# Performance work log

Measured on AMD Instinct MI355X. Metric: run time of the kernel, lower is better.

The kernel has to match this reference:

```python
import jax, jax.numpy as jnp
import numpy as np

B, T = 8, 512
N_QUBITS, N_ROT, D_PER = 64, 16, 64
D = N_QUBITS * D_PER


def setup_inputs() -> dict:
    key = jax.random.key(0)
    k1, k2, k3, k4 = jax.random.split(key, 4)
    return {
        "x": jax.random.normal(k1, (B, T, D), dtype=jnp.float32),
        "rx_params": jax.random.normal(k2, (N_QUBITS, N_ROT), dtype=jnp.float32),
        "ry_params": jax.random.normal(k3, (N_QUBITS, N_ROT), dtype=jnp.float32),
        "rz_params": jax.random.normal(k4, (N_QUBITS, N_ROT), dtype=jnp.float32),
    }


def _rot_diag(theta, axis):
    # theta: (Q,) per-qubit angle. The torch einsum 'btqd,btqq->btqd' only uses
    # the diagonal of the (Q,Q) rotation matrix. For rx/ry, the paired-qubit
    # construction puts cos(theta_k/2) on both diagonal slots of pair k
    # (first Q//2 angles are used, matching cos[..., :len(idx)]).
    Q = theta.shape[0]
    half = theta[: Q // 2] * 0.5
    if axis in ("x", "y"):
        return jnp.repeat(jnp.cos(half).astype(jnp.complex64), 2)
    # rz: diag(exp(-i a/2), exp(+i a/2)) interleaved over pairs
    e = jnp.exp(-1j * half.astype(jnp.complex64))
    return jnp.stack([e, jnp.conj(e)], axis=-1).reshape(-1)


def _apply_rotation(state, theta, axis):
    # state: (B, T, Q, d_per) complex64
    sf = jnp.fft.fft2(state, axes=(-2, -1))
    sf = sf * _rot_diag(theta, axis)[:, None]  # diagonal per-qubit scale
    return jnp.fft.ifft2(sf, axes=(-2, -1)).real  # torch takes .real


def reference(x, rx_params, ry_params, rz_params):
    b, t, d = x.shape
    q = rx_params.shape[0]
    state = x.reshape(b, t, q, d // q).astype(jnp.complex64)
    for params, axis in ((rx_params, "x"), (ry_params, "y"), (rz_params, "z")):
        theta = params.sum(-1)  # combine n_rotations into one angle per qubit
        state = _apply_rotation(state, theta, axis).astype(jnp.complex64)
    state = state.reshape(b, t, d)
    # noise model: (1 + amp_noise) * exp(i * phase_noise) * state, then L2 norm
    ka, kp = jax.random.split(jax.random.key(42))
    amp = 0.01 * jax.random.normal(ka, state.shape, dtype=jnp.float32)
    ph = 0.005 * jax.random.normal(kp, state.shape, dtype=jnp.float32)
    noisy = (1.0 + amp) * jnp.exp(1j * ph.astype(jnp.complex64)) * state
    norm = jnp.linalg.norm(noisy, axis=-1, keepdims=True)
    noisy = noisy / (norm + 1e-8)
    return jnp.abs(noisy)  # measurement
```

## Files before the change

kernel.cpp:

```cpp
#include <hip/hip_runtime.h>
#include <stdint.h>

typedef _Float16 half8 __attribute__((ext_vector_type(8)));
typedef float floatx4 __attribute__((ext_vector_type(4)));

__device__ __forceinline__ uint32_t rotl32(uint32_t v, int r) {
  return __builtin_amdgcn_alignbit(v, v, 32 - r);
}

__device__ __forceinline__ void threefry2x32(uint32_t k0, uint32_t k1,
                                             uint32_t x0, uint32_t x1,
                                             uint32_t& o0, uint32_t& o1) {
  uint32_t k2 = k0 ^ k1 ^ 0x1BD11BDAu;
  x0 += k0; x1 += k1;
#define TF_R(r) { x0 += x1; x1 = rotl32(x1, (r)); x1 ^= x0; }
  TF_R(13) TF_R(15) TF_R(26) TF_R(6)   x0 += k1; x1 += k2 + 1u;
  TF_R(17) TF_R(29) TF_R(16) TF_R(24)  x0 += k2; x1 += k0 + 2u;
  TF_R(13) TF_R(15) TF_R(26) TF_R(6)   x0 += k0; x1 += k1 + 3u;
  TF_R(17) TF_R(29) TF_R(16) TF_R(24)  x0 += k1; x1 += k2 + 4u;
  TF_R(13) TF_R(15) TF_R(26) TF_R(6)   x0 += k2; x1 += k0 + 5u;
#undef TF_R
  o0 = x0; o1 = x1;
}

__device__ __forceinline__ void threefry4x(uint32_t ka0, uint32_t ka1,
                                           const uint32_t idx[4],
                                           uint32_t bits[4]) {
  const uint32_t k2 = ka0 ^ ka1 ^ 0x1BD11BDAu;
  uint32_t x0[4], x1[4];
#pragma unroll
  for (int i = 0; i < 4; ++i) { x0[i] = ka0; x1[i] = idx[i] + ka1; }
#define TF_RND(r)                                                     \
  _Pragma("unroll") for (int i = 0; i < 4; ++i) {                     \
    x0[i] += x1[i]; x1[i] = rotl32(x1[i], (r)); x1[i] ^= x0[i];       \
  }
#define TF_INJ(a, b, c)                                               \
  _Pragma("unroll") for (int i = 0; i < 4; ++i) {                     \
    x0[i] += (a); x1[i] += (b) + (c);                                 \
  }
  TF_RND(13) TF_RND(15) TF_RND(26) TF_RND(6)   TF_INJ(ka1, k2, 1u)
  TF_RND(17) TF_RND(29) TF_RND(16) TF_RND(24)  TF_INJ(k2, ka0, 2u)
  TF_RND(13) TF_RND(15) TF_RND(26) TF_RND(6)   TF_INJ(ka0, ka1, 3u)
  TF_RND(17) TF_RND(29) TF_RND(16) TF_RND(24)  TF_INJ(ka1, k2, 4u)
  TF_RND(13) TF_RND(15) TF_RND(26) TF_RND(6)   TF_INJ(k2, ka0, 5u)
#undef TF_RND
#undef TF_INJ
#pragma unroll
  for (int i = 0; i < 4; ++i) bits[i] = x0[i] ^ x1[i];
}

__device__ __forceinline__ float tail_p(float l2) {
  float w = l2 * -0.69314718f;
  float s = sqrtf(w) - 3.0f;
  float p = -0.000200214257f;
  p = fmaf(p, s, 0.000100950558f);
  p = fmaf(p, s, 0.00134934322f);
  p = fmaf(p, s, -0.00367342844f);
  p = fmaf(p, s, 0.00573950773f);
  p = fmaf(p, s, -0.0076224613f);
  p = fmaf(p, s, 0.00943887047f);
  p = fmaf(p, s, 1.00167406f);
  p = fmaf(p, s, 2.83297682f);
  return p;
}

__device__ __forceinline__ void noise4(uint32_t ka0, uint32_t ka1,
                                       const uint32_t idx[4], float nm[4]) {
  uint32_t bits[4];
  threefry4x(ka0, ka1, idx, bits);
  float u[4], l2[4], p[4];
#pragma unroll
  for (int i = 0; i < 4; ++i) {
    float vf = __uint_as_float(__builtin_amdgcn_alignbit(0x7Fu, bits[i], 9));
    u[i] = fmaxf(fmaf(vf, 2.0f, -3.0f), -0.99999994f);
    float t = fmaf(-u[i], u[i], 1.0f);
    l2[i] = __log2f(t);
  }
#pragma unroll
  for (int i = 0; i < 4; ++i) {
    float a = fmaf(l2[i], -0.69314718f, -2.5f);
    float q = fmaf(-0.00417768164f, a, 0.246640727f);
    p[i] = fmaf(q, a, 1.50140941f);
  }
  const float lmin = fminf(fminf(l2[0], l2[1]), fminf(l2[2], l2[3]));
  if (__builtin_expect(lmin <= -7.2134752f, 0)) {
#pragma unroll
    for (int i = 0; i < 4; ++i)
      if (l2[i] <= -7.2134752f) p[i] = tail_p(l2[i]);
  }
#pragma unroll
  for (int i = 0; i < 4; ++i)
    nm[i] = fmaf(p[i], u[i] * 0.014142135623730951f, 1.0f);
}

__device__ __align__(16) _Float16 g_afrag[256 * 16];
__device__ uint32_t g_key[2];

__global__ void setup_kernel(const float* __restrict__ rx,
                             const float* __restrict__ ry,
                             const float* __restrict__ rz) {
  __shared__ float cre[3][64], cim[3][64];
  __shared__ float Gr[64], Gi[64];
  __shared__ float twc[64], tws[64];
  __shared__ float gs[64];
  const int t = threadIdx.x;

  if (t < 32) {
    const float* ps[3] = {rx, ry, rz};
    for (int a = 0; a < 3; ++a) {
      float s = 0.0f;
      for (int r = 0; r < 16; ++r) s += ps[a][t * 16 + r];
      float h = 0.5f * s;
      float ch = cosf(h), sh = sinf(h);
      if (a < 2) {
        cre[a][2 * t] = ch;     cim[a][2 * t] = 0.0f;
        cre[a][2 * t + 1] = ch; cim[a][2 * t + 1] = 0.0f;
      } else {
        cre[2][2 * t] = ch;     cim[2][2 * t] = -sh;
        cre[2][2 * t + 1] = ch; cim[2][2 * t + 1] = sh;
      }
    }
  }
  if (t < 64) {
    double ang = (2.0 * 3.14159265358979323846 / 64.0) * (double)t;
    twc[t] = (float)cos(ang);
    tws[t] = (float)sin(ang);
  }
  __syncthreads();

  if (t < 64) {
    const int k = t, kn = (64 - k) & 63;
    float pr = 1.0f, pi = 0.0f;
    for (int a = 0; a < 3; ++a) {
      float cr = 0.5f * (cre[a][k] + cre[a][kn]);
      float ci = 0.5f * (cim[a][k] - cim[a][kn]);
      float nr = pr * cr - pi * ci;
      float ni = pr * ci + pi * cr;
      pr = nr; pi = ni;
    }
    Gr[k] = pr; Gi[k] = pi;
  }
  __syncthreads();

  if (t < 64) {
    const int mi = t;
    float s = 0.0f;
    for (int k = 0; k < 64; ++k) {
      int idx = (k * mi) & 63;
      s = fmaf(Gr[k], twc[idx], s);
      s = fmaf(-Gi[k], tws[idx], s);
    }
    gs[mi] = s * (1.0f / 64.0f);
  }
  __syncthreads();

  {
    const int w = t >> 6, lane = t & 63, quad = lane >> 4, m = lane & 15;
    const int r0 = 16 * w + m - 8 * quad;
#pragma unroll
    for (int j = 0; j < 8; ++j) {
      g_afrag[t * 16 + j]     = (_Float16)gs[(r0 - j) & 63];
      g_afrag[t * 16 + 8 + j] = (_Float16)gs[(r0 - 32 - j) & 63];
    }
  }

  if (t == 0) {
    uint32_t o0, o1;
    threefry2x32(0u, 42u, 0u, 0u, o0, o1);
    g_key[0] = o0; g_key[1] = o1;
  }
}

__global__ __launch_bounds__(512, 6) void qmain(const float* __restrict__ x,
                                                float* __restrict__ out) {
  __shared__ __align__(16) _Float16 Xt[64 * 72];
  __shared__ float red[8];
  const int tid = threadIdx.x;
  const int row = blockIdx.x;
  const int lane = tid & 63;
  const int w = tid >> 6;
  const int wr = w & 3;
  const int wc = w >> 2;
  const int quad = lane >> 4;
  const int m = lane & 15;

  const half8* at = (const half8*)g_afrag;
  const int ai = (wr << 6) | lane;
  half8 af0 = at[2 * ai];
  half8 af1 = at[2 * ai + 1];
  const uint32_t ka0 = g_key[0], ka1 = g_key[1];

  {
    const float* xr = x + (size_t)row * 4096;
    const int d0 = (tid & 31) * 2;
    const int q0 = (tid >> 5) * 4;
    float2 v[4];
#pragma unroll
    for (int s = 0; s < 4; ++s) v[s] = *(const float2*)(xr + (q0 + s) * 64 + d0);
    union { _Float16 h[4]; uint2 u; } r0, r1;
#pragma unroll
    for (int s = 0; s < 4; ++s) { r0.h[s] = (_Float16)v[s].x; r1.h[s] = (_Float16)v[s].y; }
    *(uint2*)&Xt[d0 * 72 + q0] = r0.u;
    *(uint2*)&Xt[(d0 + 1) * 72 + q0] = r1.u;
  }
  __syncthreads();

  floatx4 acc[2];
#pragma unroll
  for (int cc = 0; cc < 2; ++cc) {
    const int c = 2 * wc + cc;
    const _Float16* bp = &Xt[(16 * c + m) * 72 + 8 * quad];
    half8 b0 = *(const half8*)bp;
    half8 b1 = *(const half8*)(bp + 32);
    acc[cc] = (floatx4){0.0f, 0.0f, 0.0f, 0.0f};
    acc[cc] = __builtin_amdgcn_mfma_f32_16x16x32_f16(af0, b0, acc[cc], 0, 0, 0);
    acc[cc] = __builtin_amdgcn_mfma_f32_16x16x32_f16(af1, b1, acc[cc], 0, 0, 0);
  }

  const uint32_t idxbase = ((uint32_t)row << 12) +
                           (uint32_t)(((16 * wr + 4 * quad) << 6) + (wc << 5) + m);
  float ssum = 0.0f;
#pragma unroll
  for (int g = 0; g < 2; ++g) {
    const uint32_t b = idxbase + (uint32_t)(g * 128);
    const uint32_t idx[4] = {b, b + 16u, b + 64u, b + 80u};
    float nm[4];
    noise4(ka0, ka1, idx, nm);
#pragma unroll
    for (int i = 0; i < 4; ++i) {
      const int cc = i & 1;
      const int r = g * 2 + (i >> 1);
      float val = nm[i] * acc[cc][r];
      acc[cc][r] = val;
      ssum = fmaf(val, val, ssum);
    }
  }

#pragma unroll
  for (int off = 32; off >= 1; off >>= 1) ssum += __shfl_xor(ssum, off, 64);
  if (lane == 0) red[w] = ssum;
  __syncthreads();
  float total = 0.0f;
#pragma unroll
  for (int i = 0; i < 8; ++i) total += red[i];
  const float scale = 1.0f / (sqrtf(total) + 1e-8f);

  float* ob = out + (size_t)row * 4096 +
              (size_t)(((16 * wr + 4 * quad) << 6) + (wc << 5) + m);
#pragma unroll
  for (int cc = 0; cc < 2; ++cc)
#pragma unroll
    for (int r = 0; r < 4; ++r)
      ob[r * 64 + 16 * cc] = fabsf(acc[cc][r]) * scale;
}

extern "C" void kernel_launch(void* const* d_in, const int* in_sizes, int n_in,
                              void* d_out, int out_size, void* d_ws, size_t ws_size,
                              hipStream_t stream) {
  const float* x  = (const float*)d_in[0];
  const float* rx = (const float*)d_in[1];
  const float* ry = (const float*)d_in[2];
  const float* rz = (const float*)d_in[3];
  float* out = (float*)d_out;

  setup_kernel<<<1, 256, 0, stream>>>(rx, ry, rz);
  qmain<<<4096, 512, 0, stream>>>(x, out);
}
```

Before: 138.5 us.

## Process four rows per block with double-buffered LDS prefetch of next row

Each block now handles four consecutive rows instead of one. The global load of the next row is issued before the current row's MFMA and noise work, and its result is written to a second LDS buffer so the load overlaps compute. This amortizes the per-block A-fragment and key loads and the block launch cost. In exchange it uses twice the LDS, launches only 1024 blocks (fewer waves in flight to hide latency), and relies on one barrier per iteration to order buffer reuse.

Result: slower. 142.3 us (+2.7%).

```diff
diff --git a/kernel.cpp b/kernel.cpp
--- a/kernel.cpp
+++ b/kernel.cpp
@@ -173,85 +173,108 @@
 
 __global__ __launch_bounds__(512, 6) void qmain(const float* __restrict__ x,
                                                 float* __restrict__ out) {
-  __shared__ __align__(16) _Float16 Xt[64 * 72];
-  __shared__ float red[8];
+  __shared__ __align__(16) _Float16 Xt[2][64 * 72];
+  __shared__ float red[2][8];
   const int tid = threadIdx.x;
-  const int row = blockIdx.x;
+  const int row0 = blockIdx.x << 2;
   const int lane = tid & 63;
   const int w = tid >> 6;
   const int wr = w & 3;
   const int wc = w >> 2;
   const int quad = lane >> 4;
   const int m = lane & 15;
+  const int d0 = (tid & 31) * 2;
+  const int q0 = (tid >> 5) * 4;
 
   const half8* at = (const half8*)g_afrag;
   const int ai = (wr << 6) | lane;
   half8 af0 = at[2 * ai];
   half8 af1 = at[2 * ai + 1];
   const uint32_t ka0 = g_key[0], ka1 = g_key[1];
+  const uint32_t lanebase =
+      (uint32_t)(((16 * wr + 4 * quad) << 6) + (wc << 5) + m);
 
   {
-    const float* xr = x + (size_t)row * 4096;
-    const int d0 = (tid & 31) * 2;
-    const int q0 = (tid >> 5) * 4;
+    const float* xr = x + (size_t)row0 * 4096;
     float2 v[4];
 #pragma unroll
     for (int s = 0; s < 4; ++s) v[s] = *(const float2*)(xr + (q0 + s) * 64 + d0);
     union { _Float16 h[4]; uint2 u; } r0, r1;
 #pragma unroll
     for (int s = 0; s < 4; ++s) { r0.h[s] = (_Float16)v[s].x; r1.h[s] = (_Float16)v[s].y; }
-    *(uint2*)&Xt[d0 * 72 + q0] = r0.u;
-    *(uint2*)&Xt[(d0 + 1) * 72 + q0] = r1.u;
-  }
-  __syncthreads();
-
-  floatx4 acc[2];
-#pragma unroll
-  for (int cc = 0; cc < 2; ++cc) {
-    const int c = 2 * wc + cc;
-    const _Float16* bp = &Xt[(16 * c + m) * 72 + 8 * quad];
-    half8 b0 = *(const half8*)bp;
-    half8 b1 = *(const half8*)(bp + 32);
-    acc[cc] = (floatx4){0.0f, 0.0f, 0.0f, 0.0f};
-    acc[cc] = __builtin_amdgcn_mfma_f32_16x16x32_f16(af0, b0, acc[cc], 0, 0, 0);
-    acc[cc] = __builtin_amdgcn_mfma_f32_16x16x32_f16(af1, b1, acc[cc], 0, 0, 0);
-  }
-
-  const uint32_t idxbase = ((uint32_t)row << 12) +
-                           (uint32_t)(((16 * wr + 4 * quad) << 6) + (wc << 5) + m);
-  float ssum = 0.0f;
-#pragma unroll
-  for (int g = 0; g < 2; ++g) {
-    const uint32_t b = idxbase + (uint32_t)(g * 128);
-    const uint32_t idx[4] = {b, b + 16u, b + 64u, b + 80u};
-    float nm[4];
-    noise4(ka0, ka1, idx, nm);
-#pragma unroll
-    for (int i = 0; i < 4; ++i) {
-      const int cc = i & 1;
-      const int r = g * 2 + (i >> 1);
-      float val = nm[i] * acc[cc][r];
-      acc[cc][r] = val;
-      ssum = fmaf(val, val, ssum);
-    }
-  }
-
-#pragma unroll
-  for (int off = 32; off >= 1; off >>= 1) ssum += __shfl_xor(ssum, off, 64);
-  if (lane == 0) red[w] = ssum;
-  __syncthreads();
-  float total = 0.0f;
-#pragma unroll
-  for (int i = 0; i < 8; ++i) total += red[i];
-  const float scale = 1.0f / (sqrtf(total) + 1e-8f);
-
-  float* ob = out + (size_t)row * 4096 +
-              (size_t)(((16 * wr + 4 * quad) << 6) + (wc << 5) + m);
-#pragma unroll
-  for (int cc = 0; cc < 2; ++cc)
-#pragma unroll
-    for (int r = 0; r < 4; ++r)
-      ob[r * 64 + 16 * cc] = fabsf(acc[cc][r]) * scale;
+    *(uint2*)&Xt[0][d0 * 72 + q0] = r0.u;
+    *(uint2*)&Xt[0][(d0 + 1) * 72 + q0] = r1.u;
+  }
+  __syncthreads();
+
+#pragma unroll
+  for (int it = 0; it < 4; ++it) {
+    const int cur = it & 1;
+    const int row = row0 + it;
+
+    float2 v[4];
+    if (it < 3) {
+      const float* xr = x + (size_t)(row + 1) * 4096;
+#pragma unroll
+      for (int s = 0; s < 4; ++s)
+        v[s] = *(const float2*)(xr + (q0 + s) * 64 + d0);
+    }
+
+    floatx4 acc[2];
+#pragma unroll
+    for (int cc = 0; cc < 2; ++cc) {
+      const int c = 2 * wc + cc;
+      const _Float16* bp = &Xt[cur][(16 * c + m) * 72 + 8 * quad];
+      half8 b0 = *(const half8*)bp;
+      half8 b1 = *(const half8*)(bp + 32);
+      acc[cc] = (floatx4){0.0f, 0.0f, 0.0f, 0.0f};
+      acc[cc] = __builtin_amdgcn_mfma_f32_16x16x32_f16(af0, b0, acc[cc], 0, 0, 0);
+      acc[cc] = __builtin_amdgcn_mfma_f32_16x16x32_f16(af1, b1, acc[cc], 0, 0, 0);
+    }
+
+    if (it < 3) {
+      union { _Float16 h[4]; uint2 u; } r0, r1;
+#pragma unroll
+      for (int s = 0; s < 4; ++s) { r0.h[s] = (_Float16)v[s].x; r1.h[s] = (_Float16)v[s].y; }
+      *(uint2*)&Xt[cur ^ 1][d0 * 72 + q0] = r0.u;
+      *(uint2*)&Xt[cur ^ 1][(d0 + 1) * 72 + q0] = r1.u;
+    }
+
+    const uint32_t idxbase = ((uint32_t)row << 12) + lanebase;
+    float ssum = 0.0f;
+#pragma unroll
+    for (int g = 0; g < 2; ++g) {
+      const uint32_t b = idxbase + (uint32_t)(g * 128);
+      const uint32_t idx[4] = {b, b + 16u, b + 64u, b + 80u};
+      float nm[4];
+      noise4(ka0, ka1, idx, nm);
+#pragma unroll
+      for (int i = 0; i < 4; ++i) {
+        const int cc = i & 1;
+        const int r = g * 2 + (i >> 1);
+        float val = nm[i] * acc[cc][r];
+        acc[cc][r] = val;
+        ssum = fmaf(val, val, ssum);
+      }
+    }
+
+#pragma unroll
+    for (int off = 32; off >= 1; off >>= 1) ssum += __shfl_xor(ssum, off, 64);
+    if (lane == 0) red[cur][w] = ssum;
+    __syncthreads();
+
+    float total = 0.0f;
+#pragma unroll
+    for (int i = 0; i < 8; ++i) total += red[cur][i];
+    const float scale = 1.0f / (sqrtf(total) + 1e-8f);
+
+    float* ob = out + (size_t)row * 4096 + (size_t)lanebase;
+#pragma unroll
+    for (int cc = 0; cc < 2; ++cc)
+#pragma unroll
+      for (int r = 0; r < 4; ++r)
+        ob[r * 64 + 16 * cc] = fabsf(acc[cc][r]) * scale;
+  }
 }
 
 extern "C" void kernel_launch(void* const* d_in, const int* in_sizes, int n_in,
@@ -264,5 +287,5 @@
   float* out = (float*)d_out;
 
   setup_kernel<<<1, 256, 0, stream>>>(rx, ry, rz);
-  qmain<<<4096, 512, 0, stream>>>(x, out);
-}
+  qmain<<<1024, 512, 0, stream>>>(x, out);
+}
```
